# Performance work log

Measured on AMD Instinct MI355X. Metric: run time of the kernel, lower is better.

## Reference

```python
import jax, jax.numpy as jnp
import numpy as np


def _uniform_directions(key, num_thetas, d):
    # dect.generate_uniform_directions: gaussian columns normalized to unit norm, shape [d, T]
    v = jax.random.normal(key, (d, num_thetas), dtype=jnp.float32)
    return v / jnp.linalg.norm(v, axis=0, keepdims=True)


def _compute_ect(x, v, radius, resolution, scale):
    # x: [N, d], v: [d, T] -> nh: [N, T] projections of points onto directions
    nh = x @ v
    # thresholds: [R, 1, 1]
    lin = jnp.linspace(-radius, radius, resolution, dtype=x.dtype)[:, None, None]
    # scaled sigmoid of (threshold - projection), broadcast to [R, N, T]
    ecc = jax.nn.sigmoid(scale * (lin - nh))
    # Euler characteristic curve: sum over points -> [R, T]
    return ecc.sum(axis=1)


def setup_inputs() -> dict:
    key = jax.random.key(0)
    k1, k2 = jax.random.split(key)
    space1 = jax.random.normal(k1, (384, 128), dtype=jnp.float32)
    space2 = jax.random.normal(k2, (384, 32), dtype=jnp.float32)
    return {"space1": space1, "space2": space2}


def reference(space1, space2):
    n1, d1 = space1.shape
    n2, d2 = space2.shape
    RADIUS = 1.0
    SCALE = 500.0
    # directions generated deterministically (seed 42 in original) per space dims
    v1 = _uniform_directions(jax.random.key(42), n1, d1)
    v2 = _uniform_directions(jax.random.key(42), n2, d2)
    input_ect = _compute_ect(space1, v1, RADIUS, n1, SCALE)   # [n1, n1]
    latent_ect = _compute_ect(space2, v2, RADIUS, n2, SCALE)  # [n2, n2]
    # MSELoss (mean reduction)
    loss = jnp.mean((input_ect - latent_ect) ** 2)
    return loss
```

## Files before the change

kernel.cpp:

```cpp
#include <hip/hip_runtime.h>
#include <hip/hip_bf16.h>
#include <stdint.h>

#define TT 384
#define NN 384
#define RR 384
#define D1 128
#define D2 32

#define THETA 0.0352f
#define HALF_SLOTS 191.5f
#define BAND_ITERS 14

__device__ inline void threefry2x32(uint32_t k0, uint32_t k1,
                                    uint32_t x0, uint32_t x1,
                                    uint32_t& o0, uint32_t& o1) {
    uint32_t ks2 = k0 ^ k1 ^ 0x1BD11BDAu;
    x0 += k0; x1 += k1;
    #define TF_ROUND(r) { x0 += x1; x1 = (x1 << (r)) | (x1 >> (32 - (r))); x1 ^= x0; }
    TF_ROUND(13) TF_ROUND(15) TF_ROUND(26) TF_ROUND(6)
    x0 += k1;  x1 += ks2 + 1u;
    TF_ROUND(17) TF_ROUND(29) TF_ROUND(16) TF_ROUND(24)
    x0 += ks2; x1 += k0 + 2u;
    TF_ROUND(13) TF_ROUND(15) TF_ROUND(26) TF_ROUND(6)
    x0 += k0;  x1 += k1 + 3u;
    TF_ROUND(17) TF_ROUND(29) TF_ROUND(16) TF_ROUND(24)
    x0 += k1;  x1 += ks2 + 4u;
    TF_ROUND(13) TF_ROUND(15) TF_ROUND(26) TF_ROUND(6)
    x0 += ks2; x1 += k0 + 5u;
    #undef TF_ROUND
    o0 = x0; o1 = x1;
}

__device__ inline float erfinv_f32(float x) {
    float w = -log1pf(-x * x);
    float p;
    if (w < 5.0f) {
        w = w - 2.5f;
        p =            2.81022636e-08f;
        p = fmaf(p, w, 3.43273939e-07f);
        p = fmaf(p, w, -3.5233877e-06f);
        p = fmaf(p, w, -4.39150654e-06f);
        p = fmaf(p, w, 0.00021858087f);
        p = fmaf(p, w, -0.00125372503f);
        p = fmaf(p, w, -0.00417768164f);
        p = fmaf(p, w, 0.246640727f);
        p = fmaf(p, w, 1.50140941f);
    } else {
        w = sqrtf(w) - 3.0f;
        p =            -0.000200214257f;
        p = fmaf(p, w, 0.000100950558f);
        p = fmaf(p, w, 0.00134934322f);
        p = fmaf(p, w, -0.00367342844f);
        p = fmaf(p, w, 0.00573950773f);
        p = fmaf(p, w, -0.0076224613f);
        p = fmaf(p, w, 0.00943887047f);
        p = fmaf(p, w, 1.00167406f);
        p = fmaf(p, w, 2.83297682f);
    }
    return p * x;
}

__device__ inline float bits_to_normal(uint32_t bits) {
    uint32_t fb = (bits >> 9) | 0x3F800000u;
    float f = __uint_as_float(fb) - 1.0f;
    float lo = __uint_as_float(0xBF7FFFFFu);
    float u = f * 2.0f + lo;
    u = fmaxf(lo, u);
    return 1.41421356237f * erfinv_f32(u);
}

__global__ void prep_kernel(float* __restrict__ xT1, float* __restrict__ xT2,
                            const float* __restrict__ x1, const float* __restrict__ x2,
                            float* __restrict__ out) {
    int idx = blockIdx.x * 256 + threadIdx.x;
    if (idx == 0) out[0] = 0.0f;
    if (idx < D1 * TT) {
        int k = idx / NN, n = idx % NN;
        xT1[idx] = x1[n * D1 + k];
    } else {
        int idx2 = idx - D1 * TT;
        if (idx2 < D2 * TT) {
            int k = idx2 / NN, n = idx2 % NN;
            xT2[idx2] = x2[n * D2 + k];
        }
    }
}

__device__ inline void scatter_point(float p, float sgn,
                                     float* __restrict__ inc,
                                     float* __restrict__ band) {
    int r1  = (int)ceilf((p + (1.0f + THETA)) * HALF_SLOTS);
    int rlo = (int)ceilf((p + (1.0f - THETA)) * HALF_SLOTS);
    if (r1 <= 0)        atomicAdd(&inc[0], sgn);
    else if (r1 <= 383) atomicAdd(&inc[r1], sgn);
    #pragma unroll
    for (int j = 0; j < BAND_ITERS; ++j) {
        int r = rlo + j;
        if (r >= 0 && r < r1 && r < RR) {
            float lin = -1.0f + 2.0f * (float)r / 383.0f;
            float sig = __builtin_amdgcn_rcpf(1.0f + __expf(500.0f * (p - lin)));
            atomicAdd(&band[r], sgn * sig);
        }
    }
}

__global__ void __launch_bounds__(384) ect_fused(
        const float* __restrict__ xT1, const float* __restrict__ xT2,
        float* __restrict__ out) {
    int t = blockIdx.x;
    int tid = threadIdx.x;
    int lane = tid & 63;
    int w = tid >> 6;
    __shared__ float v1s[D1];
    __shared__ float v2s[D2];
    __shared__ float inc[RR];
    __shared__ float band[RR];
    __shared__ float red[8];

    float g = 0.0f;
    if (tid < D1 + D2) {
        int i = (tid < D1) ? tid : tid - D1;
        uint32_t flat = (uint32_t)i * TT + (uint32_t)t;
        uint32_t o0, o1;
        threefry2x32(0u, 42u, 0u, flat, o0, o1);
        g = bits_to_normal(o0 ^ o1);
    }
    float sq = g * g;
    #pragma unroll
    for (int off = 32; off > 0; off >>= 1) sq += __shfl_xor(sq, off, 64);
    if (lane == 0) red[w] = sq;
    __syncthreads();
    float nrm1 = sqrtf(red[0] + red[1]);
    float nrm2 = sqrtf(red[2]);
    if (tid < D1)           v1s[tid] = g / nrm1;
    else if (tid < D1 + D2) v2s[tid - D1] = g / nrm2;
    inc[tid] = 0.0f;
    band[tid] = 0.0f;
    __syncthreads();

    int n = tid;
    float p1 = 0.0f, p2 = 0.0f;
    #pragma unroll 8
    for (int k = 0; k < D1; ++k) p1 = fmaf(xT1[k * NN + n], v1s[k], p1);
    #pragma unroll 8
    for (int k = 0; k < D2; ++k) p2 = fmaf(xT2[k * NN + n], v2s[k], p2);

    scatter_point(p1,  1.0f, inc, band);
    scatter_point(p2, -1.0f, inc, band);
    __syncthreads();

    float v = inc[tid];
    #pragma unroll
    for (int s = 1; s < 64; s <<= 1) {
        float u = __shfl_up(v, s, 64);
        if (lane >= s) v += u;
    }
    if (lane == 63) red[w] = v;
    __syncthreads();
    float off_acc = 0.0f;
    for (int j = 0; j < w; ++j) off_acc += red[j];
    v += off_acc;

    float d = v + band[tid];
    float s2 = d * d;
    #pragma unroll
    for (int off = 32; off > 0; off >>= 1) s2 += __shfl_xor(s2, off, 64);
    __syncthreads();
    if (lane == 0) red[w] = s2;
    __syncthreads();
    if (tid == 0) {
        float s = red[0] + red[1] + red[2] + red[3] + red[4] + red[5];
        atomicAdd(out, s * (1.0f / ((float)RR * (float)TT)));
    }
}

extern "C" void kernel_launch(void* const* d_in, const int* in_sizes, int n_in,
                              void* d_out, int out_size, void* d_ws, size_t ws_size,
                              hipStream_t stream) {
    const float* space1 = (const float*)d_in[0];
    const float* space2 = (const float*)d_in[1];
    float* out = (float*)d_out;

    float* ws = (float*)d_ws;
    float* xT1 = ws;
    float* xT2 = xT1 + D1 * TT;

    prep_kernel<<<240, 256, 0, stream>>>(xT1, xT2, space1, space2, out);
    ect_fused<<<TT, 384, 0, stream>>>(xT1, xT2, out);
}
```

Before: 86.80 us.

## Drop transpose prep kernel and project rows directly with float4 loads

```diff
diff --git a/kernel.cpp b/kernel.cpp
--- a/kernel.cpp
+++ b/kernel.cpp
@@ -1,5 +1,4 @@
 #include <hip/hip_runtime.h>
-#include <hip/hip_bf16.h>
 #include <stdint.h>
 
 #define TT 384
@@ -70,21 +69,8 @@
     return 1.41421356237f * erfinv_f32(u);
 }
 
-__global__ void prep_kernel(float* __restrict__ xT1, float* __restrict__ xT2,
-                            const float* __restrict__ x1, const float* __restrict__ x2,
-                            float* __restrict__ out) {
-    int idx = blockIdx.x * 256 + threadIdx.x;
-    if (idx == 0) out[0] = 0.0f;
-    if (idx < D1 * TT) {
-        int k = idx / NN, n = idx % NN;
-        xT1[idx] = x1[n * D1 + k];
-    } else {
-        int idx2 = idx - D1 * TT;
-        if (idx2 < D2 * TT) {
-            int k = idx2 / NN, n = idx2 % NN;
-            xT2[idx2] = x2[n * D2 + k];
-        }
-    }
+__global__ void zero_out_k(float* __restrict__ out) {
+    if (threadIdx.x == 0) out[0] = 0.0f;
 }
 
 __device__ inline void scatter_point(float p, float sgn,
@@ -106,7 +92,7 @@
 }
 
 __global__ void __launch_bounds__(384) ect_fused(
-        const float* __restrict__ xT1, const float* __restrict__ xT2,
+        const float* __restrict__ x1, const float* __restrict__ x2,
         float* __restrict__ out) {
     int t = blockIdx.x;
     int tid = threadIdx.x;
@@ -139,12 +125,38 @@
     band[tid] = 0.0f;
     __syncthreads();
 
-    int n = tid;
+    const float4* __restrict__ x1v = (const float4*)x1;
+    const float4* __restrict__ x2v = (const float4*)x2;
+    float4 vf1 = *(const float4*)&v1s[4 * (lane & 31)];
+    float4 vf2 = *(const float4*)&v2s[4 * (lane & 7)];
+
     float p1 = 0.0f, p2 = 0.0f;
+
+    int base1 = (w * 64 + (lane >> 5)) * 32 + (lane & 31);
     #pragma unroll 8
-    for (int k = 0; k < D1; ++k) p1 = fmaf(xT1[k * NN + n], v1s[k], p1);
-    #pragma unroll 8
-    for (int k = 0; k < D2; ++k) p2 = fmaf(xT2[k * NN + n], v2s[k], p2);
+    for (int j = 0; j < 32; ++j) {
+        float4 xv = x1v[base1 + 64 * j];
+        float s = xv.x * vf1.x;
+        s = fmaf(xv.y, vf1.y, s);
+        s = fmaf(xv.z, vf1.z, s);
+        s = fmaf(xv.w, vf1.w, s);
+        #pragma unroll
+        for (int m = 16; m > 0; m >>= 1) s += __shfl_xor(s, m, 64);
+        if ((lane & 31) == j) p1 = s;
+    }
+
+    int base2 = (w * 64 + (lane >> 3)) * 8 + (lane & 7);
+    #pragma unroll
+    for (int j = 0; j < 8; ++j) {
+        float4 xv = x2v[base2 + 64 * j];
+        float s = xv.x * vf2.x;
+        s = fmaf(xv.y, vf2.y, s);
+        s = fmaf(xv.z, vf2.z, s);
+        s = fmaf(xv.w, vf2.w, s);
+        #pragma unroll
+        for (int m = 4; m > 0; m >>= 1) s += __shfl_xor(s, m, 64);
+        if ((lane & 7) == j) p2 = s;
+    }
 
     scatter_point(p1,  1.0f, inc, band);
     scatter_point(p2, -1.0f, inc, band);
@@ -182,10 +194,8 @@
     const float* space2 = (const float*)d_in[1];
     float* out = (float*)d_out;
 
-    float* ws = (float*)d_ws;
-    float* xT1 = ws;
-    float* xT2 = xT1 + D1 * TT;
-
-    prep_kernel<<<240, 256, 0, stream>>>(xT1, xT2, space1, space2, out);
-    ect_fused<<<TT, 384, 0, stream>>>(xT1, xT2, out);
-}
+    (void)d_ws; (void)ws_size;
+
+    zero_out_k<<<1, 64, 0, stream>>>(out);
+    ect_fused<<<TT, 384, 0, stream>>>(space1, space2, out);
+}
```

After: 84.51 us. -2.6%, faster.
